# Optimization experiments

Measured on AMD Instinct MI355X. Metric: run time of the kernel, lower is better.

## Reference

```python
import jax, jax.numpy as jnp
import numpy as np

BN_EPS = 1e-5
SAMPLE_KEY = jax.random.key(42)


def setup_inputs() -> dict:
    key = jax.random.key(0)
    ks = jax.random.split(key, 12)
    B, W, E = 524288, 8, 4
    D = W * E  # 32, input dim of fc1

    def lin(k, fan_in, fan_out):
        k1, k2 = jax.random.split(k)
        bound = 1.0 / np.sqrt(fan_in)
        w = jax.random.uniform(k1, (fan_in, fan_out), jnp.float32, -bound, bound)
        b = jax.random.uniform(k2, (fan_out,), jnp.float32, -bound, bound)
        return w, b

    W1, b1 = lin(ks[0], D, 50)
    W2, b2 = lin(ks[1], 50, 30)
    W3, b3 = lin(ks[2], 30, 20)
    W4, b4 = lin(ks[3], 20, 15)
    W5, b5 = lin(ks[4], 15, W)
    # BatchNorm affine params (eval mode, running_mean=0, running_var=1)
    g1, be1 = jnp.ones((50,), jnp.float32), jnp.zeros((50,), jnp.float32)
    g2, be2 = jnp.ones((30,), jnp.float32), jnp.zeros((30,), jnp.float32)
    g3, be3 = jnp.ones((20,), jnp.float32), jnp.zeros((20,), jnp.float32)
    events = jax.random.normal(ks[5], (B, W, E), jnp.float32)
    return {"events": events,
            "W1": W1, "b1": b1, "g1": g1, "be1": be1,
            "W2": W2, "b2": b2, "g2": g2, "be2": be2,
            "W3": W3, "b3": b3, "g3": g3, "be3": be3,
            "W4": W4, "b4": b4, "W5": W5, "b5": b5}


def _bn_eval(x, g, b):
    # eval-mode BatchNorm1d with running_mean=0, running_var=1
    return x * (g / jnp.sqrt(1.0 + BN_EPS)) + b


def _probs(events, W1, b1, g1, be1, W2, b2, g2, be2, W3, b3, g3, be3, W4, b4, W5, b5):
    B = events.shape[0]
    x = events.reshape(B, -1)  # (B, window*event_size)
    h = jax.nn.relu(_bn_eval(x @ W1 + b1, g1, be1))
    h = jax.nn.relu(_bn_eval(h @ W2 + b2, g2, be2))
    h = jax.nn.relu(_bn_eval(h @ W3 + b3, g3, be3))
    h = jax.nn.relu(h @ W4 + b4)
    return jax.nn.sigmoid(h @ W5 + b5)  # (B, window_size)


def reference(events, W1, b1, g1, be1, W2, b2, g2, be2, W3, b3, g3, be3, W4, b4, W5, b5):
    p = _probs(events, W1, b1, g1, be1, W2, b2, g2, be2, W3, b3, g3, be3, W4, b4, W5, b5)
    # np.random.choice([0,1], p=[p, 1-p]) => P(choice=1) = 1 - p
    choice = jax.random.bernoulli(SAMPLE_KEY, 1.0 - p).astype(p.dtype)  # (B, W)
    chosen_events_np = 1.0 - choice
    flipped = jnp.abs(choice - p)            # prob of sampled outcome per element
    log_prob = jnp.log(jnp.prod(flipped, axis=1))  # (B,)
    return chosen_events_np, log_prob
```

## Files before the change

kernel.cpp:

```cpp
#include <hip/hip_runtime.h>
#include <math.h>

#define THREADS 256
#define TPW 8
#define ROWS_PER_BLOCK 512
#define P_MARGIN 2e-4f
#define FIXCAP 64

typedef float f32x4 __attribute__((ext_vector_type(4)));
typedef short short8 __attribute__((ext_vector_type(8)));
union Frag { unsigned u[4]; short8 s; };

#define FR1 0
#define FR2 2048
#define FR3 4096
#define FR4 5120
#define FR5 5632
#define VB1 6144
#define VS1 6208
#define VE1 6272
#define VB2 6336
#define VS2 6368
#define VE2 6400
#define VB3 6432
#define VS3 6464
#define VE3 6496
#define VB4 6528
#define VB5 6544
#define ZEND 6560
#define ACT 6560
#define PT  10912
#define WPOOL 11488

__device__ __forceinline__ void tf2x32(unsigned x0, unsigned x1,
                                       unsigned &o0, unsigned &o1) {
  const unsigned k0 = 0u;
  const unsigned k1 = 42u;
  const unsigned k2 = 0x1BD11BDAu ^ k0 ^ k1;
  x0 += k0; x1 += k1;
#define TF_R(r) { x0 += x1; x1 = (x1 << (r)) | (x1 >> (32 - (r))); x1 ^= x0; }
  TF_R(13) TF_R(15) TF_R(26) TF_R(6)
  x0 += k1; x1 += k2 + 1u;
  TF_R(17) TF_R(29) TF_R(16) TF_R(24)
  x0 += k2; x1 += k0 + 2u;
  TF_R(13) TF_R(15) TF_R(26) TF_R(6)
  x0 += k0; x1 += k1 + 3u;
  TF_R(17) TF_R(29) TF_R(16) TF_R(24)
  x0 += k1; x1 += k2 + 4u;
  TF_R(13) TF_R(15) TF_R(26) TF_R(6)
  x0 += k2; x1 += k0 + 5u;
#undef TF_R
  o0 = x0; o1 = x1;
}

__device__ __forceinline__ unsigned rtnb(float v) {
  unsigned b = __float_as_uint(v);
  return (b + 0x7FFFu + ((b >> 16) & 1u)) & 0xFFFF0000u;
}

__device__ __forceinline__ unsigned cvtpk(float a, float b) {
  unsigned r;
  asm("v_cvt_pk_bf16_f32 %0, %1, %2" : "=v"(r) : "v"(a), "v"(b));
  return r;
}

__device__ __forceinline__ void pack8(const float f[8], short8 &H, short8 &L) {
  Frag h, l;
#pragma unroll
  for (int d = 0; d < 4; ++d) {
    unsigned hd = cvtpk(f[2 * d], f[2 * d + 1]);
    h.u[d] = hd;
    float r0 = f[2 * d]     - __uint_as_float(hd << 16);
    float r1 = f[2 * d + 1] - __uint_as_float(hd & 0xFFFF0000u);
    l.u[d] = cvtpk(r0, r1);
  }
  H = h.s; L = l.s;
}

__device__ __forceinline__ f32x4 mfma16(short8 a, short8 b, f32x4 c) {
  return __builtin_amdgcn_mfma_f32_16x16x32_bf16(a, b, c, 0, 0, 0);
}

__device__ __forceinline__ short8 ldfrag(const float *sW, int dwoff) {
  return *reinterpret_cast<const short8 *>(sW + dwoff);
}

template <int K, int N, int NT, int FB>
__device__ __forceinline__ void stage_layer(const float *__restrict__ W,
                                            float *sW, int t) {
  for (int i = t; i < K * N; i += THREADS) {
    int k = i / N, c = i - k * N;
    float v = W[i];
    unsigned hb = rtnb(v);
    float lov = v - __uint_as_float(hb);
    unsigned lb = rtnb(lov);
    int kt = k >> 5, gg = (k >> 3) & 3, d = (k >> 1) & 3, par = k & 1;
    int nt = c >> 4, lane = gg * 16 + (c & 15);
    int combo = kt * NT + nt;
    int dwhi = FB + (combo * 2 + 0) * 256 + lane * 4 + d;
    unsigned short *hp = reinterpret_cast<unsigned short *>(sW);
    hp[2 * dwhi + par] = (unsigned short)(hb >> 16);
    hp[2 * (dwhi + 256) + par] = (unsigned short)(lb >> 16);
  }
}

__device__ __forceinline__ void loadA(const float *actw, int kbase, int c,
                                      int g, short8 &H, short8 &L) {
  float f[8];
#pragma unroll
  for (int e = 0; e < 8; ++e) f[e] = actw[(kbase + g * 8 + e) * 17 + c];
  pack8(f, H, L);
}

__global__ __launch_bounds__(THREADS, 2)
void wtf_kernel(const float* __restrict__ events,
                const float* __restrict__ W1, const float* __restrict__ b1,
                const float* __restrict__ g1, const float* __restrict__ be1,
                const float* __restrict__ W2, const float* __restrict__ b2,
                const float* __restrict__ g2, const float* __restrict__ be2,
                const float* __restrict__ W3, const float* __restrict__ b3,
                const float* __restrict__ g3, const float* __restrict__ be3,
                const float* __restrict__ W4, const float* __restrict__ b4,
                const float* __restrict__ W5, const float* __restrict__ b5,
                float* __restrict__ out_chosen,
                float* __restrict__ out_logp,
                int B) {
  __shared__ float sW[WPOOL];
  __shared__ unsigned s_cnt;
  __shared__ unsigned s_rows[FIXCAP];
  __shared__ double sA[64];
  __shared__ double sB[64];
  __shared__ double sF[8];

  const int t = threadIdx.x;
  const float rden = (float)(1.0 / sqrt(1.0 + 1e-5));

  if (t == 0) s_cnt = 0;
  for (int i = t; i < ZEND; i += THREADS) sW[i] = 0.f;
  __syncthreads();
  stage_layer<32, 50, 4, FR1>(W1, sW, t);
  stage_layer<50, 30, 2, FR2>(W2, sW, t);
  stage_layer<30, 20, 2, FR3>(W3, sW, t);
  stage_layer<20, 15, 1, FR4>(W4, sW, t);
  stage_layer<15, 8, 1, FR5>(W5, sW, t);
  if (t < 50)                  { sW[VB1 + t] = b1[t]; sW[VS1 + t] = g1[t] * rden; sW[VE1 + t] = be1[t]; }
  else if (t >= 64 && t < 94)  { int i = t - 64;  sW[VB2 + i] = b2[i]; sW[VS2 + i] = g2[i] * rden; sW[VE2 + i] = be2[i]; }
  else if (t >= 128 && t < 148){ int i = t - 128; sW[VB3 + i] = b3[i]; sW[VS3 + i] = g3[i] * rden; sW[VE3 + i] = be3[i]; }
  else if (t >= 192 && t < 207){ sW[VB4 + (t - 192)] = b4[t - 192]; }
  else if (t >= 224 && t < 232){ sW[VB5 + (t - 224)] = b5[t - 224]; }
  __syncthreads();

  const int w = t >> 6, lane = t & 63;
  const int c = lane & 15, g = lane >> 4;
  float *actw = sW + ACT + w * 1088;
  float *ptw  = sW + PT  + w * 144;

#pragma unroll 1
  for (int tt = 0; tt < TPW; ++tt) {
    const int r0 = blockIdx.x * ROWS_PER_BLOCK + w * (TPW * 16) + tt * 16;

    const float4 *xr = reinterpret_cast<const float4 *>(
        events + (size_t)(r0 + c) * 32 + g * 8);
    float4 xa = xr[0], xb = xr[1];
    float xf[8] = {xa.x, xa.y, xa.z, xa.w, xb.x, xb.y, xb.z, xb.w};
    short8 Xh, Xl; pack8(xf, Xh, Xl);

    {
      f32x4 acc[4];
#pragma unroll
      for (int nt = 0; nt < 4; ++nt) {
        float bb = sW[VB1 + nt * 16 + c];
        f32x4 ci = {bb, bb, bb, bb};
        short8 bh = ldfrag(sW, FR1 + (nt * 2 + 0) * 256 + lane * 4);
        short8 bl = ldfrag(sW, FR1 + (nt * 2 + 1) * 256 + lane * 4);
        ci = mfma16(Xl, bh, ci);
        ci = mfma16(Xh, bl, ci);
        acc[nt] = mfma16(Xh, bh, ci);
      }
#pragma unroll
      for (int nt = 0; nt < 4; ++nt) {
        float sc = sW[VS1 + nt * 16 + c], of = sW[VE1 + nt * 16 + c];
#pragma unroll
        for (int r = 0; r < 4; ++r)
          actw[(nt * 16 + c) * 17 + g * 4 + r] =
              fmaxf(fmaf(acc[nt][r], sc, of), 0.f);
      }
    }

    {
      f32x4 acc[2];
#pragma unroll
      for (int nt = 0; nt < 2; ++nt) {
        float bb = sW[VB2 + nt * 16 + c];
        acc[nt] = f32x4{bb, bb, bb, bb};
      }
#pragma unroll
      for (int kt = 0; kt < 2; ++kt) {
        short8 Ah, Al; loadA(actw, kt * 32, c, g, Ah, Al);
#pragma unroll
        for (int nt = 0; nt < 2; ++nt) {
          short8 bh = ldfrag(sW, FR2 + ((kt * 2 + nt) * 2 + 0) * 256 + lane * 4);
          short8 bl = ldfrag(sW, FR2 + ((kt * 2 + nt) * 2 + 1) * 256 + lane * 4);
          acc[nt] = mfma16(Al, bh, acc[nt]);
          acc[nt] = mfma16(Ah, bl, acc[nt]);
          acc[nt] = mfma16(Ah, bh, acc[nt]);
        }
      }
#pragma unroll
      for (int nt = 0; nt < 2; ++nt) {
        float sc = sW[VS2 + nt * 16 + c], of = sW[VE2 + nt * 16 + c];
#pragma unroll
        for (int r = 0; r < 4; ++r)
          actw[(nt * 16 + c) * 17 + g * 4 + r] =
              fmaxf(fmaf(acc[nt][r], sc, of), 0.f);
      }
    }

    {
      f32x4 acc[2];
#pragma unroll
      for (int nt = 0; nt < 2; ++nt) {
        float bb = sW[VB3 + nt * 16 + c];
        acc[nt] = f32x4{bb, bb, bb, bb};
      }
      short8 Ah, Al; loadA(actw, 0, c, g, Ah, Al);
#pragma unroll
      for (int nt = 0; nt < 2; ++nt) {
        short8 bh = ldfrag(sW, FR3 + (nt * 2 + 0) * 256 + lane * 4);
        short8 bl = ldfrag(sW, FR3 + (nt * 2 + 1) * 256 + lane * 4);
        acc[nt] = mfma16(Al, bh, acc[nt]);
        acc[nt] = mfma16(Ah, bl, acc[nt]);
        acc[nt] = mfma16(Ah, bh, acc[nt]);
      }
#pragma unroll
      for (int nt = 0; nt < 2; ++nt) {
        float sc = sW[VS3 + nt * 16 + c], of = sW[VE3 + nt * 16 + c];
#pragma unroll
        for (int r = 0; r < 4; ++r)
          actw[(nt * 16 + c) * 17 + g * 4 + r] =
              fmaxf(fmaf(acc[nt][r], sc, of), 0.f);
      }
    }

    {
      float bb = sW[VB4 + c];
      f32x4 acc = {bb, bb, bb, bb};
      short8 Ah, Al; loadA(actw, 0, c, g, Ah, Al);
      short8 bh = ldfrag(sW, FR4 + 0 * 256 + lane * 4);
      short8 bl = ldfrag(sW, FR4 + 1 * 256 + lane * 4);
      acc = mfma16(Al, bh, acc);
      acc = mfma16(Ah, bl, acc);
      acc = mfma16(Ah, bh, acc);
#pragma unroll
      for (int r = 0; r < 4; ++r) {
        actw[c * 17 + g * 4 + r] = fmaxf(acc[r], 0.f);
        actw[(16 + c) * 17 + g * 4 + r] = 0.f;
      }
    }

    {
      float bb = sW[VB5 + c];
      f32x4 acc = {bb, bb, bb, bb};
      short8 Ah, Al; loadA(actw, 0, c, g, Ah, Al);
      short8 bh = ldfrag(sW, FR5 + 0 * 256 + lane * 4);
      short8 bl = ldfrag(sW, FR5 + 1 * 256 + lane * 4);
      acc = mfma16(Al, bh, acc);
      acc = mfma16(Ah, bl, acc);
      acc = mfma16(Ah, bh, acc);
      if (c < 8) {
#pragma unroll
        for (int r = 0; r < 4; ++r) ptw[(g * 4 + r) * 9 + c] = acc[r];
      }
    }

    {
      const int erow = lane >> 2, cp = lane & 3;
      const int grow = r0 + erow;
      float l0 = ptw[erow * 9 + 2 * cp];
      float l1 = ptw[erow * 9 + 2 * cp + 1];
      float p0 = 1.f / (1.f + __expf(-l0));
      float p1 = 1.f / (1.f + __expf(-l1));
      unsigned o0, o1, q0, q1;
      tf2x32(0u, 8u * (unsigned)grow + 2u * cp,      o0, o1);
      tf2x32(0u, 8u * (unsigned)grow + 2u * cp + 1u, q0, q1);
      float u0 = __uint_as_float(0x3F800000u | ((o0 ^ o1) >> 9)) - 1.f;
      float u1 = __uint_as_float(0x3F800000u | ((q0 ^ q1) >> 9)) - 1.f;
      float th0 = 1.f - p0, th1 = 1.f - p1;
      bool c0 = u0 < th0, c1 = u1 < th1;
      bool need = (fabsf(u0 - th0) < P_MARGIN) || (fabsf(u1 - th1) < P_MARGIN);
      float prod = (c0 ? th0 : p0) * (c1 ? th1 : p1);
      prod *= __shfl_xor(prod, 1);
      prod *= __shfl_xor(prod, 2);
      float2 chv = make_float2(c0 ? 0.f : 1.f, c1 ? 0.f : 1.f);
      *reinterpret_cast<float2 *>(out_chosen + (size_t)grow * 8 + 2 * cp) = chv;
      if (cp == 0) out_logp[grow] = __logf(prod);
      if (need) {
        unsigned i = atomicAdd(&s_cnt, 1u);
        if (i < FIXCAP) s_rows[i] = (unsigned)grow;
      }
    }
  }

  __syncthreads();
  unsigned cnt = s_cnt;
  if (cnt > FIXCAP) cnt = FIXCAP;
  if (cnt == 0) return;

  const double denom = sqrt(1.0 + 1e-5);
  for (unsigned r = 0; r < cnt; ++r) {
    const int rb = (int)s_rows[r];

    if (t < 32) sA[t] = (double)events[(size_t)rb * 32 + t];
    __syncthreads();

    double v = 0.0;
    if (t < 50) {
#pragma unroll
      for (int k = 0; k < 32; ++k) v = fma(sA[k], (double)W1[k * 50 + t], v);
      v += (double)b1[t];
      v = v * ((double)g1[t] / denom) + (double)be1[t];
      v = v > 0.0 ? v : 0.0;
    }
    __syncthreads();
    if (t < 50) sB[t] = v;
    __syncthreads();

    v = 0.0;
    if (t < 30) {
#pragma unroll
      for (int k = 0; k < 50; ++k) v = fma(sB[k], (double)W2[k * 30 + t], v);
      v += (double)b2[t];
      v = v * ((double)g2[t] / denom) + (double)be2[t];
      v = v > 0.0 ? v : 0.0;
    }
    __syncthreads();
    if (t < 30) sA[t] = v;
    __syncthreads();

    v = 0.0;
    if (t < 20) {
#pragma unroll
      for (int k = 0; k < 30; ++k) v = fma(sA[k], (double)W3[k * 20 + t], v);
      v += (double)b3[t];
      v = v * ((double)g3[t] / denom) + (double)be3[t];
      v = v > 0.0 ? v : 0.0;
    }
    __syncthreads();
    if (t < 20) sB[t] = v;
    __syncthreads();

    v = 0.0;
    if (t < 15) {
#pragma unroll
      for (int k = 0; k < 20; ++k) v = fma(sB[k], (double)W4[k * 15 + t], v);
      v += (double)b4[t];
      v = v > 0.0 ? v : 0.0;
    }
    __syncthreads();
    if (t < 15) sA[t] = v;
    __syncthreads();

    if (t < 8) {
      v = 0.0;
#pragma unroll
      for (int k = 0; k < 15; ++k) v = fma(sA[k], (double)W5[k * 8 + t], v);
      v += (double)b5[t];
      double p = 1.0 / (1.0 + exp(-v));
      unsigned j = 8u * (unsigned)rb + (unsigned)t, o0, o1;
      tf2x32(0u, j, o0, o1);
      unsigned bits = o0 ^ o1;
      float u = __uint_as_float(0x3F800000u | (bits >> 9)) - 1.f;
      double thr = 1.0 - p;
      bool choice = ((double)u < thr);
      out_chosen[(size_t)rb * 8 + t] = choice ? 0.f : 1.f;
      sF[t] = choice ? thr : p;
    }
    __syncthreads();
    if (t == 0) {
      double prod = 1.0;
      for (int w2 = 0; w2 < 8; ++w2) prod *= sF[w2];
      out_logp[rb] = (float)log(prod);
    }
    __syncthreads();
  }
}

extern "C" void kernel_launch(void* const* d_in, const int* in_sizes, int n_in,
                              void* d_out, int out_size, void* d_ws, size_t ws_size,
                              hipStream_t stream) {
  const float* events = (const float*)d_in[0];
  const float* W1  = (const float*)d_in[1];
  const float* b1  = (const float*)d_in[2];
  const float* g1  = (const float*)d_in[3];
  const float* be1 = (const float*)d_in[4];
  const float* W2  = (const float*)d_in[5];
  const float* b2  = (const float*)d_in[6];
  const float* g2  = (const float*)d_in[7];
  const float* be2 = (const float*)d_in[8];
  const float* W3  = (const float*)d_in[9];
  const float* b3  = (const float*)d_in[10];
  const float* g3  = (const float*)d_in[11];
  const float* be3 = (const float*)d_in[12];
  const float* W4  = (const float*)d_in[13];
  const float* b4  = (const float*)d_in[14];
  const float* W5  = (const float*)d_in[15];
  const float* b5  = (const float*)d_in[16];

  const int B = in_sizes[0] / 32;
  float* out = (float*)d_out;
  float* out_chosen = out;
  float* out_logp   = out + (size_t)B * 8;

  const int blocks = (B + ROWS_PER_BLOCK - 1) / ROWS_PER_BLOCK;
  hipLaunchKernelGGL(wtf_kernel, dim3(blocks), dim3(THREADS), 0, stream,
                     events, W1, b1, g1, be1, W2, b2, g2, be2,
                     W3, b3, g3, be3, W4, b4, W5, b5,
                     out_chosen, out_logp, B);
}
```

Before: 230.9 us.

## Shrink LDS footprint, keep small-layer weights in registers, prefetch next tile input

Halves rows per block and tiles per wave, and packs the bias and scale vectors tightly. The layer-4/5 weight fragments are staged into the activation scratch, loaded into registers once, then overwritten, and the fallback double buffers alias that same region, which reduces LDS per block and should allow more resident blocks. The next tile's event rows are prefetched during the current tile to hide global load latency. The costs are more blocks, with the weight staging repeated per block, and extra register pressure from the held fragments and the prefetch.

```diff
diff --git a/kernel.cpp b/kernel.cpp
--- a/kernel.cpp
+++ b/kernel.cpp
@@ -2,8 +2,8 @@
 #include <math.h>
 
 #define THREADS 256
-#define TPW 8
-#define ROWS_PER_BLOCK 512
+#define TPW 4
+#define ROWS_PER_BLOCK 256
 #define P_MARGIN 2e-4f
 #define FIXCAP 64
 
@@ -14,23 +14,21 @@
 #define FR1 0
 #define FR2 2048
 #define FR3 4096
-#define FR4 5120
-#define FR5 5632
-#define VB1 6144
-#define VS1 6208
-#define VE1 6272
-#define VB2 6336
-#define VS2 6368
-#define VE2 6400
-#define VB3 6432
-#define VS3 6464
-#define VE3 6496
-#define VB4 6528
-#define VB5 6544
-#define ZEND 6560
-#define ACT 6560
-#define PT  10912
-#define WPOOL 11488
+#define VB1 5120
+#define VS1 5170
+#define VE1 5220
+#define VB2 5270
+#define VS2 5300
+#define VE2 5330
+#define VB3 5360
+#define VS3 5380
+#define VE3 5400
+#define VB4 5420
+#define VB5 5435
+#define ACT 5460
+#define WPOOL (ACT + 4 * 1088)
+#define FRT4 ACT
+#define FRT5 (ACT + 512)
 
 __device__ __forceinline__ void tf2x32(unsigned x0, unsigned x1,
                                        unsigned &o0, unsigned &o1) {
@@ -128,21 +126,18 @@
   __shared__ float sW[WPOOL];
   __shared__ unsigned s_cnt;
   __shared__ unsigned s_rows[FIXCAP];
-  __shared__ double sA[64];
-  __shared__ double sB[64];
-  __shared__ double sF[8];
 
   const int t = threadIdx.x;
   const float rden = (float)(1.0 / sqrt(1.0 + 1e-5));
 
   if (t == 0) s_cnt = 0;
-  for (int i = t; i < ZEND; i += THREADS) sW[i] = 0.f;
+  for (int i = t; i < ACT + 1024; i += THREADS) sW[i] = 0.f;
   __syncthreads();
   stage_layer<32, 50, 4, FR1>(W1, sW, t);
   stage_layer<50, 30, 2, FR2>(W2, sW, t);
   stage_layer<30, 20, 2, FR3>(W3, sW, t);
-  stage_layer<20, 15, 1, FR4>(W4, sW, t);
-  stage_layer<15, 8, 1, FR5>(W5, sW, t);
+  stage_layer<20, 15, 1, FRT4>(W4, sW, t);
+  stage_layer<15, 8, 1, FRT5>(W5, sW, t);
   if (t < 50)                  { sW[VB1 + t] = b1[t]; sW[VS1 + t] = g1[t] * rden; sW[VE1 + t] = be1[t]; }
   else if (t >= 64 && t < 94)  { int i = t - 64;  sW[VB2 + i] = b2[i]; sW[VS2 + i] = g2[i] * rden; sW[VE2 + i] = be2[i]; }
   else if (t >= 128 && t < 148){ int i = t - 128; sW[VB3 + i] = b3[i]; sW[VS3 + i] = g3[i] * rden; sW[VE3 + i] = be3[i]; }
@@ -152,18 +147,29 @@
 
   const int w = t >> 6, lane = t & 63;
   const int c = lane & 15, g = lane >> 4;
+
+  const short8 bh4 = ldfrag(sW, FRT4 + lane * 4);
+  const short8 bl4 = ldfrag(sW, FRT4 + 256 + lane * 4);
+  const short8 bh5 = ldfrag(sW, FRT5 + lane * 4);
+  const short8 bl5 = ldfrag(sW, FRT5 + 256 + lane * 4);
+  __syncthreads();
+
   float *actw = sW + ACT + w * 1088;
-  float *ptw  = sW + PT  + w * 144;
+  float *ptw  = actw + 544;
+
+  const int wrow0 = blockIdx.x * ROWS_PER_BLOCK + w * (TPW * 16);
+  const float4 *xp = reinterpret_cast<const float4 *>(
+      events + (size_t)(wrow0 + c) * 32 + g * 8);
+  float4 xa = xp[0], xb = xp[1];
 
 #pragma unroll 1
   for (int tt = 0; tt < TPW; ++tt) {
-    const int r0 = blockIdx.x * ROWS_PER_BLOCK + w * (TPW * 16) + tt * 16;
-
-    const float4 *xr = reinterpret_cast<const float4 *>(
-        events + (size_t)(r0 + c) * 32 + g * 8);
-    float4 xa = xr[0], xb = xr[1];
+    const int r0 = wrow0 + tt * 16;
+
     float xf[8] = {xa.x, xa.y, xa.z, xa.w, xb.x, xb.y, xb.z, xb.w};
     short8 Xh, Xl; pack8(xf, Xh, Xl);
+    const int ttn = (tt + 1 < TPW) ? tt + 1 : tt;
+    xa = xp[ttn * 128]; xb = xp[ttn * 128 + 1];
 
     {
       f32x4 acc[4];
@@ -246,11 +252,9 @@
       float bb = sW[VB4 + c];
       f32x4 acc = {bb, bb, bb, bb};
       short8 Ah, Al; loadA(actw, 0, c, g, Ah, Al);
-      short8 bh = ldfrag(sW, FR4 + 0 * 256 + lane * 4);
-      short8 bl = ldfrag(sW, FR4 + 1 * 256 + lane * 4);
-      acc = mfma16(Al, bh, acc);
-      acc = mfma16(Ah, bl, acc);
-      acc = mfma16(Ah, bh, acc);
+      acc = mfma16(Al, bh4, acc);
+      acc = mfma16(Ah, bl4, acc);
+      acc = mfma16(Ah, bh4, acc);
 #pragma unroll
       for (int r = 0; r < 4; ++r) {
         actw[c * 17 + g * 4 + r] = fmaxf(acc[r], 0.f);
@@ -262,11 +266,9 @@
       float bb = sW[VB5 + c];
       f32x4 acc = {bb, bb, bb, bb};
       short8 Ah, Al; loadA(actw, 0, c, g, Ah, Al);
-      short8 bh = ldfrag(sW, FR5 + 0 * 256 + lane * 4);
-      short8 bl = ldfrag(sW, FR5 + 1 * 256 + lane * 4);
-      acc = mfma16(Al, bh, acc);
-      acc = mfma16(Ah, bl, acc);
-      acc = mfma16(Ah, bh, acc);
+      acc = mfma16(Al, bh5, acc);
+      acc = mfma16(Ah, bl5, acc);
+      acc = mfma16(Ah, bh5, acc);
       if (c < 8) {
 #pragma unroll
         for (int r = 0; r < 4; ++r) ptw[(g * 4 + r) * 9 + c] = acc[r];
@@ -306,6 +308,10 @@
   if (cnt > FIXCAP) cnt = FIXCAP;
   if (cnt == 0) return;
 
+  double *sA = reinterpret_cast<double *>(sW + ACT);
+  double *sB = sA + 64;
+  double *sF = sB + 64;
+
   const double denom = sqrt(1.0 + 1e-5);
   for (unsigned r = 0; r < cnt; ++r) {
     const int rb = (int)s_rows[r];
```

Result: faster. 223.8 us (-3.0%).
